# Kernel optimization log

Measured on AMD Instinct MI355X. Metric: run time of the kernel, lower is better.

## Reference

```python
import jax, jax.numpy as jnp
import numpy as np

N, H, E, G, OUT = 50000, 128, 600000, 256, 64
NUM_ITERS = 5
GAMMA = 0.1
EPS = 0.1
NEG_SLOPE = 0.01


def setup_inputs() -> dict:
    key = jax.random.key(0)
    ks = jax.random.split(key, 10)
    s = 1.0 / np.sqrt(H)
    x = jax.random.normal(ks[0], (N, H), dtype=jnp.float32)
    edge_index = jax.random.randint(ks[1], (2, E), 0, N, dtype=jnp.int64)
    batch = jnp.sort(jax.random.randint(ks[2], (N,), 0, G, dtype=jnp.int64))
    W = jax.random.normal(ks[3], (H, H), dtype=jnp.float32) * s
    bias = jax.random.normal(ks[4], (H,), dtype=jnp.float32) * s
    lin_w = jax.random.normal(ks[5], (H, H), dtype=jnp.float32) * s
    l1_w = jax.random.normal(ks[6], (3 * H // 2, 3 * H), dtype=jnp.float32) / np.sqrt(3 * H)
    l1_b = jax.random.normal(ks[7], (3 * H // 2,), dtype=jnp.float32) * 0.01
    l2_w = jax.random.normal(ks[8], (OUT, 3 * H // 2), dtype=jnp.float32) / np.sqrt(3 * H // 2)
    l2_b = jax.random.normal(ks[9], (OUT,), dtype=jnp.float32) * 0.01
    return {"x": x, "edge_index": edge_index, "batch": batch, "W": W, "bias": bias,
            "lin_w": lin_w, "l1_w": l1_w, "l1_b": l1_b, "l2_w": l2_w, "l2_b": l2_b}


def reference(x, edge_index, batch, W, bias, lin_w, l1_w, l1_b, l2_w, l2_b):
    n = x.shape[0]
    src, dst = edge_index[0], edge_index[1]
    # antisymmetric weight: W - W^T - gamma*I
    A = W - W.T - GAMMA * jnp.eye(W.shape[0], dtype=x.dtype)
    for _ in range(NUM_ITERS):
        neigh = x @ lin_w.T                                   # [N,H] linear (no bias)
        agg = jax.ops.segment_sum(neigh[src], dst, num_segments=n)  # gather-scatter add
        conv = x @ A.T + agg + bias
        x = x + EPS * jnp.tanh(conv)
    # triple global pooling per graph: add / max / mean
    add = jax.ops.segment_sum(x, batch, num_segments=G)
    mx = jax.ops.segment_max(x, batch, num_segments=G)
    cnt = jax.ops.segment_sum(jnp.ones((n,), dtype=x.dtype), batch, num_segments=G)
    safe_cnt = jnp.maximum(cnt, 1.0)[:, None]
    mean = add / safe_cnt
    mx = jnp.where(cnt[:, None] > 0, mx, 0.0)
    pooled = jnp.concatenate([add, mx, mean], axis=1)          # [G, 3H]
    h = jax.nn.leaky_relu(pooled @ l1_w.T + l1_b, NEG_SLOPE)
    out = jax.nn.leaky_relu(h @ l2_w.T + l2_b, NEG_SLOPE)
    return out
```

## Files before the change

kernel.cpp:

```cpp
#include <hip/hip_runtime.h>
#include <hip/hip_fp16.h>
#include <cmath>

#define H 128
#define GAMMA 0.1f
#define EPS 0.1f
#define NEG 0.01f
#define NGRAPH 256

typedef _Float16 half_t;
typedef _Float16 f16x8 __attribute__((ext_vector_type(8)));
typedef _Float16 f16x4 __attribute__((ext_vector_type(4)));
typedef _Float16 f16x2 __attribute__((ext_vector_type(2)));
typedef float f32x4 __attribute__((ext_vector_type(4)));

__device__ __forceinline__ float fast_tanh(float v) {
    float e = __builtin_amdgcn_exp2f(v * 2.8853900817779268f);
    float r = __builtin_amdgcn_rcpf(e + 1.0f);
    return 1.0f - 2.0f * r;
}

__global__ __launch_bounds__(256) void prep_cast_zero(
        const float* __restrict__ W, const float* __restrict__ lin_w,
        half_t* __restrict__ WtTf, const float* __restrict__ x,
        half_t* __restrict__ xh, int n4, int* __restrict__ deg, int N) {
    int stride = gridDim.x * 256;
    int tot = max(n4, max(32768, N));
    for (int i = blockIdx.x * 256 + threadIdx.x; i < tot; i += stride) {
        if (i < n4) {
            float4 v = *(const float4*)(x + (size_t)i * 4);
            half_t* o = xh + (size_t)i * 4;
            o[0] = (half_t)v.x; o[1] = (half_t)v.y; o[2] = (half_t)v.z; o[3] = (half_t)v.w;
        }
        if (i < 32768) {
            int t = i & 7;
            int lane = (i >> 3) & 63;
            int ct = (i >> 9) & 7;
            int s = i >> 12;
            int q = lane >> 4, m = lane & 15;
            int j = m * 8 + ct;
            int k = s * 32 + q * 8 + t;
            float v;
            if (k < H) v = W[j * H + k] - W[k * H + j] - (j == k ? GAMMA : 0.f);
            else       v = lin_w[j * H + (k - H)];
            WtTf[i] = (half_t)v;
        }
        if (i < N) deg[i] = 0;
    }
}

__global__ __launch_bounds__(256) void count_kernel(const int* __restrict__ dst,
                                                    int* __restrict__ deg, int E) {
    int stride = gridDim.x * 256;
    for (int e = blockIdx.x * 256 + threadIdx.x; e < E; e += stride)
        atomicAdd(&deg[dst[e]], 1);
}

#define SCHUNK 2048
__global__ __launch_bounds__(256) void scan_part(const int* __restrict__ deg,
                                                 int* __restrict__ partials, int N) {
    __shared__ int red[256];
    int t = threadIdx.x, b = blockIdx.x;
    int base = b * SCHUNK + t * 8;
    int s = 0;
#pragma unroll
    for (int i = 0; i < 8; ++i) { int idx = base + i; if (idx < N) s += deg[idx]; }
    red[t] = s;
    __syncthreads();
    for (int off = 128; off > 0; off >>= 1) {
        if (t < off) red[t] += red[t + off];
        __syncthreads();
    }
    if (t == 0) partials[b] = red[0];
}

__global__ void scan_mid(const int* __restrict__ partials, int* __restrict__ blkoff, int nblk) {
    int lane = threadIdx.x;
    int p = (lane < nblk) ? partials[lane] : 0;
    int v = p;
    for (int off = 1; off < 64; off <<= 1) {
        int u = __shfl_up(v, off);
        if (lane >= off) v += u;
    }
    if (lane < nblk) blkoff[lane] = v - p;
}

__global__ __launch_bounds__(256) void scan_final(const int* __restrict__ deg,
        const int* __restrict__ blkoff, int* __restrict__ row_start,
        int* __restrict__ cursor, int N, int E) {
    __shared__ int red[256];
    int t = threadIdx.x, b = blockIdx.x;
    int base = b * SCHUNK + t * 8;
    int v[8]; int s = 0;
#pragma unroll
    for (int i = 0; i < 8; ++i) { int idx = base + i; v[i] = (idx < N) ? deg[idx] : 0; s += v[i]; }
    red[t] = s;
    __syncthreads();
    for (int off = 1; off < 256; off <<= 1) {
        int u = (t >= off) ? red[t - off] : 0;
        __syncthreads();
        red[t] += u;
        __syncthreads();
    }
    int run = blkoff[b] + red[t] - s;
#pragma unroll
    for (int i = 0; i < 8; ++i) {
        int idx = base + i;
        if (idx < N) { row_start[idx] = run; cursor[idx] = run; run += v[i]; }
    }
    if (b == 0 && t == 0) row_start[N] = E;
}

__global__ __launch_bounds__(256) void fill_kernel(const int* __restrict__ src,
        const int* __restrict__ dst, int* __restrict__ cursor,
        int* __restrict__ csr_src, int E) {
    int stride = gridDim.x * 256;
    for (int e = blockIdx.x * 256 + threadIdx.x; e < E; e += stride) {
        int p = atomicAdd(&cursor[dst[e]], 1);
        csr_src[p] = src[e];
    }
}

__global__ __launch_bounds__(256) void gather_agg(const half_t* __restrict__ xh,
        const int* __restrict__ row_start, const int* __restrict__ csr_src,
        half_t* __restrict__ xaggh, int N) {
    int wid = __builtin_amdgcn_readfirstlane(blockIdx.x * 4 + (threadIdx.x >> 6));
    int nwaves = gridDim.x * 4;
    int lane = threadIdx.x & 63;
    for (int node = wid; node < N; node += nwaves) {
        int begin = row_start[node];
        int end   = row_start[node + 1];
        f16x2 accA = (f16x2){(half_t)0.f, (half_t)0.f};
        f16x2 accB = (f16x2){(half_t)0.f, (half_t)0.f};
        for (int base = begin; base < end; base += 64) {
            int cnt = min(64, end - base);
            int myidx = csr_src[base + min(lane, cnt - 1)];
            int j = 0;
            for (; j + 7 < cnt; j += 8) {
                int s0 = __builtin_amdgcn_readlane(myidx, j + 0);
                int s1 = __builtin_amdgcn_readlane(myidx, j + 1);
                int s2 = __builtin_amdgcn_readlane(myidx, j + 2);
                int s3 = __builtin_amdgcn_readlane(myidx, j + 3);
                int s4 = __builtin_amdgcn_readlane(myidx, j + 4);
                int s5 = __builtin_amdgcn_readlane(myidx, j + 5);
                int s6 = __builtin_amdgcn_readlane(myidx, j + 6);
                int s7 = __builtin_amdgcn_readlane(myidx, j + 7);
                f16x2 v0 = *(const f16x2*)(xh + (size_t)s0 * H + lane * 2);
                f16x2 v1 = *(const f16x2*)(xh + (size_t)s1 * H + lane * 2);
                f16x2 v2 = *(const f16x2*)(xh + (size_t)s2 * H + lane * 2);
                f16x2 v3 = *(const f16x2*)(xh + (size_t)s3 * H + lane * 2);
                f16x2 v4 = *(const f16x2*)(xh + (size_t)s4 * H + lane * 2);
                f16x2 v5 = *(const f16x2*)(xh + (size_t)s5 * H + lane * 2);
                f16x2 v6 = *(const f16x2*)(xh + (size_t)s6 * H + lane * 2);
                f16x2 v7 = *(const f16x2*)(xh + (size_t)s7 * H + lane * 2);
                accA += v0; accB += v1; accA += v2; accB += v3;
                accA += v4; accB += v5; accA += v6; accB += v7;
            }
            if (cnt - j >= 4) {
                int s0 = __builtin_amdgcn_readlane(myidx, j + 0);
                int s1 = __builtin_amdgcn_readlane(myidx, j + 1);
                int s2 = __builtin_amdgcn_readlane(myidx, j + 2);
                int s3 = __builtin_amdgcn_readlane(myidx, j + 3);
                f16x2 v0 = *(const f16x2*)(xh + (size_t)s0 * H + lane * 2);
                f16x2 v1 = *(const f16x2*)(xh + (size_t)s1 * H + lane * 2);
                f16x2 v2 = *(const f16x2*)(xh + (size_t)s2 * H + lane * 2);
                f16x2 v3 = *(const f16x2*)(xh + (size_t)s3 * H + lane * 2);
                accA += v0; accB += v1; accA += v2; accB += v3;
                j += 4;
            }
            int rem = cnt - j;
            if (rem > 0) {
                int s0 = __builtin_amdgcn_readlane(myidx, j);
                int s1 = __builtin_amdgcn_readlane(myidx, min(j + 1, cnt - 1));
                int s2 = __builtin_amdgcn_readlane(myidx, min(j + 2, cnt - 1));
                f16x2 v0 = *(const f16x2*)(xh + (size_t)s0 * H + lane * 2);
                f16x2 v1 = *(const f16x2*)(xh + (size_t)s1 * H + lane * 2);
                f16x2 v2 = *(const f16x2*)(xh + (size_t)s2 * H + lane * 2);
                accA += v0;
                if (rem > 1) accB += v1;
                if (rem > 2) accA += v2;
            }
        }
        f16x2 o = accA + accB;
        *(f16x2*)(xaggh + (size_t)node * H + lane * 2) = o;
    }
}

#define CROWS 64
__global__ __launch_bounds__(256) void conv_mfma(
        const half_t* __restrict__ xh, const half_t* __restrict__ xaggh,
        const half_t* __restrict__ WtTf, const float* __restrict__ bias,
        half_t* __restrict__ xhout, int N) {
    int tid = threadIdx.x;
    int wave = tid >> 6, lane = tid & 63;
    int q = lane >> 4, m = lane & 15;
    int n0 = blockIdx.x * CROWS + wave * 16;

    f32x4 acc[8];
#pragma unroll
    for (int ct = 0; ct < 8; ++ct) acc[ct] = (f32x4){0.f, 0.f, 0.f, 0.f};

    int arow = min(n0 + m, N - 1);
#pragma unroll
    for (int s = 0; s < 8; ++s) {
        f16x8 afrag = (s < 4)
            ? *(const f16x8*)(xh    + (size_t)arow * H + s * 32 + q * 8)
            : *(const f16x8*)(xaggh + (size_t)arow * H + (s - 4) * 32 + q * 8);
#pragma unroll
        for (int ct = 0; ct < 8; ++ct) {
            f16x8 bfrag = *(const f16x8*)(WtTf + ((s * 8 + ct) * 64 + lane) * 8);
            acc[ct] = __builtin_amdgcn_mfma_f32_16x16x32_f16(afrag, bfrag, acc[ct], 0, 0, 0);
        }
    }

    float4 b0 = *(const float4*)(bias + m * 8);
    float4 b1 = *(const float4*)(bias + m * 8 + 4);
    float bb[8] = {b0.x, b0.y, b0.z, b0.w, b1.x, b1.y, b1.z, b1.w};
#pragma unroll
    for (int r = 0; r < 4; ++r) {
        int row = n0 + q * 4 + r;
        if (row < N) {
            f16x8 xr = *(const f16x8*)(xh + (size_t)row * H + m * 8);
            f16x8 o;
#pragma unroll
            for (int ct = 0; ct < 8; ++ct) {
                float c = acc[ct][r] + bb[ct];
                o[ct] = (half_t)((float)xr[ct] + EPS * fast_tanh(c));
            }
            *(f16x8*)(xhout + (size_t)row * H + m * 8) = o;
        }
    }
}

__global__ __launch_bounds__(1024) void pool_mlp(const half_t* __restrict__ x,
        const int* __restrict__ batch,
        const float* __restrict__ l1_w, const float* __restrict__ l1_b,
        const float* __restrict__ l2_w, const float* __restrict__ l2_b,
        float* __restrict__ out, int N) {
    __shared__ float ssum[8][128];
    __shared__ float smax[8][128];
    __shared__ __align__(16) float sp[384];
    __shared__ __align__(16) float sh[192];
    int g = blockIdx.x, t = threadIdx.x;
    int feat = t & 127, slot = t >> 7;
    int lo = 0, hi = N;
    while (lo < hi) { int mid = (lo + hi) >> 1; if (batch[mid] < g) lo = mid + 1; else hi = mid; }
    int start = lo;
    hi = N;
    while (lo < hi) { int mid = (lo + hi) >> 1; if (batch[mid] < g + 1) lo = mid + 1; else hi = mid; }
    int end = lo;
    float sum = 0.f, mx = -INFINITY;
    for (int n = start + slot; n < end; n += 8) {
        float v = (float)x[(size_t)n * H + feat];
        sum += v;
        mx = fmaxf(mx, v);
    }
    ssum[slot][feat] = sum;
    smax[slot][feat] = mx;
    __syncthreads();
    if (t < 128) {
        float s = 0.f, m = -INFINITY;
#pragma unroll
        for (int k = 0; k < 8; ++k) { s += ssum[k][t]; m = fmaxf(m, smax[k][t]); }
        int cnt = end - start;
        sp[t] = s;
        sp[128 + t] = (cnt > 0) ? m : 0.f;
        sp[256 + t] = s / (float)(cnt > 0 ? cnt : 1);
    }
    __syncthreads();
    if (t < 192) {
        float acc = l1_b[t];
        const float* wr = l1_w + (size_t)t * 384;
        for (int k = 0; k < 384; k += 4) {
            float4 w = *(const float4*)(wr + k);
            float4 p = *(const float4*)(sp + k);
            acc += w.x * p.x + w.y * p.y + w.z * p.z + w.w * p.w;
        }
        sh[t] = acc > 0.f ? acc : NEG * acc;
    }
    __syncthreads();
    if (t < 64) {
        float acc = l2_b[t];
        const float* wr = l2_w + (size_t)t * 192;
        for (int k = 0; k < 192; k += 4) {
            float4 w = *(const float4*)(wr + k);
            float4 p = *(const float4*)(sh + k);
            acc += w.x * p.x + w.y * p.y + w.z * p.z + w.w * p.w;
        }
        out[g * 64 + t] = acc > 0.f ? acc : NEG * acc;
    }
}

extern "C" void kernel_launch(void* const* d_in, const int* in_sizes, int n_in,
                              void* d_out, int out_size, void* d_ws, size_t ws_size,
                              hipStream_t stream) {
    const float* x0    = (const float*)d_in[0];
    const int*   edge  = (const int*)d_in[1];
    const int*   batch = (const int*)d_in[2];
    const float* W     = (const float*)d_in[3];
    const float* bias  = (const float*)d_in[4];
    const float* lin_w = (const float*)d_in[5];
    const float* l1_w  = (const float*)d_in[6];
    const float* l1_b  = (const float*)d_in[7];
    const float* l2_w  = (const float*)d_in[8];
    const float* l2_b  = (const float*)d_in[9];
    float* out = (float*)d_out;

    int N = in_sizes[0] / H;
    int E = in_sizes[1] / 2;
    const int* src = edge;
    const int* dst = edge + E;

    size_t nh = (size_t)N * H;
    half_t* xhA    = (half_t*)d_ws;
    half_t* xhB    = xhA + nh;
    half_t* xaggh  = xhB + nh;
    half_t* WtTf   = xaggh + nh;
    int* deg       = (int*)(WtTf + 32768);
    int* row_start = deg + N;
    int* cursor    = row_start + N + 1;
    int* csr_src   = cursor + N;
    int* partials  = csr_src + E;
    int* blkoff    = partials + 64;

    int n4 = (int)(nh / 4);
    prep_cast_zero<<<1024, 256, 0, stream>>>(W, lin_w, WtTf, x0, xhA, n4, deg, N);

    count_kernel<<<1024, 256, 0, stream>>>(dst, deg, E);
    int nblk = (N + SCHUNK - 1) / SCHUNK;
    scan_part<<<nblk, 256, 0, stream>>>(deg, partials, N);
    scan_mid<<<1, 64, 0, stream>>>(partials, blkoff, nblk);
    scan_final<<<nblk, 256, 0, stream>>>(deg, blkoff, row_start, cursor, N, E);
    fill_kernel<<<1024, 256, 0, stream>>>(src, dst, cursor, csr_src, E);

    const half_t* xcur_h = xhA;
    int nblocks = (N + CROWS - 1) / CROWS;
    for (int it = 0; it < 5; ++it) {
        gather_agg<<<2048, 256, 0, stream>>>(xcur_h, row_start, csr_src, xaggh, N);
        half_t* xnext_h = (it & 1) ? xhA : xhB;
        conv_mfma<<<nblocks, 256, 0, stream>>>(xcur_h, xaggh, WtTf, bias, xnext_h, N);
        xcur_h = xnext_h;
    }

    pool_mlp<<<NGRAPH, 1024, 0, stream>>>(xcur_h, batch, l1_w, l1_b, l2_w, l2_b, out, N);
}
```

Measured before the change: 372.5 us.

## Fuse neighbor gather-aggregation into conv MFMA kernel via LDS staging

The separate gather_agg kernel is folded into the conv kernel. Each wave now aggregates neighbor rows for its own 16 nodes into a swizzled LDS tile, and the MFMA A-fragments for the aggregate half are read from that tile. This removes the global round trip for xaggh and one launch per iteration. In exchange, gather parallelism is tied to the conv grid of 782 blocks, with each wave processing its 16 nodes one after another, which may hide memory latency less well. Separately, the scan_mid kernel is removed and each scan_final block computes its own block offset with a wave reduction over the partials.

```diff
diff --git a/kernel.cpp b/kernel.cpp
--- a/kernel.cpp
+++ b/kernel.cpp
@@ -74,22 +74,17 @@
     if (t == 0) partials[b] = red[0];
 }
 
-__global__ void scan_mid(const int* __restrict__ partials, int* __restrict__ blkoff, int nblk) {
-    int lane = threadIdx.x;
-    int p = (lane < nblk) ? partials[lane] : 0;
-    int v = p;
-    for (int off = 1; off < 64; off <<= 1) {
-        int u = __shfl_up(v, off);
-        if (lane >= off) v += u;
-    }
-    if (lane < nblk) blkoff[lane] = v - p;
-}
-
 __global__ __launch_bounds__(256) void scan_final(const int* __restrict__ deg,
-        const int* __restrict__ blkoff, int* __restrict__ row_start,
+        const int* __restrict__ partials, int* __restrict__ row_start,
         int* __restrict__ cursor, int N, int E) {
     __shared__ int red[256];
+    __shared__ int s_boff;
     int t = threadIdx.x, b = blockIdx.x;
+    if (t < 64) {
+        int p = (t < b) ? partials[t] : 0;
+        for (int off = 32; off > 0; off >>= 1) p += __shfl_down(p, off);
+        if (t == 0) s_boff = p;
+    }
     int base = b * SCHUNK + t * 8;
     int v[8]; int s = 0;
 #pragma unroll
@@ -102,7 +97,7 @@
         red[t] += u;
         __syncthreads();
     }
-    int run = blkoff[b] + red[t] - s;
+    int run = s_boff + red[t] - s;
 #pragma unroll
     for (int i = 0; i < 8; ++i) {
         int idx = base + i;
@@ -121,80 +116,79 @@
     }
 }
 
-__global__ __launch_bounds__(256) void gather_agg(const half_t* __restrict__ xh,
+#define CROWS 64
+__global__ __launch_bounds__(256) void conv_fused(
+        const half_t* __restrict__ xh,
         const int* __restrict__ row_start, const int* __restrict__ csr_src,
-        half_t* __restrict__ xaggh, int N) {
-    int wid = __builtin_amdgcn_readfirstlane(blockIdx.x * 4 + (threadIdx.x >> 6));
-    int nwaves = gridDim.x * 4;
-    int lane = threadIdx.x & 63;
-    for (int node = wid; node < N; node += nwaves) {
-        int begin = row_start[node];
-        int end   = row_start[node + 1];
-        f16x2 accA = (f16x2){(half_t)0.f, (half_t)0.f};
-        f16x2 accB = (f16x2){(half_t)0.f, (half_t)0.f};
-        for (int base = begin; base < end; base += 64) {
-            int cnt = min(64, end - base);
-            int myidx = csr_src[base + min(lane, cnt - 1)];
-            int j = 0;
-            for (; j + 7 < cnt; j += 8) {
-                int s0 = __builtin_amdgcn_readlane(myidx, j + 0);
-                int s1 = __builtin_amdgcn_readlane(myidx, j + 1);
-                int s2 = __builtin_amdgcn_readlane(myidx, j + 2);
-                int s3 = __builtin_amdgcn_readlane(myidx, j + 3);
-                int s4 = __builtin_amdgcn_readlane(myidx, j + 4);
-                int s5 = __builtin_amdgcn_readlane(myidx, j + 5);
-                int s6 = __builtin_amdgcn_readlane(myidx, j + 6);
-                int s7 = __builtin_amdgcn_readlane(myidx, j + 7);
-                f16x2 v0 = *(const f16x2*)(xh + (size_t)s0 * H + lane * 2);
-                f16x2 v1 = *(const f16x2*)(xh + (size_t)s1 * H + lane * 2);
-                f16x2 v2 = *(const f16x2*)(xh + (size_t)s2 * H + lane * 2);
-                f16x2 v3 = *(const f16x2*)(xh + (size_t)s3 * H + lane * 2);
-                f16x2 v4 = *(const f16x2*)(xh + (size_t)s4 * H + lane * 2);
-                f16x2 v5 = *(const f16x2*)(xh + (size_t)s5 * H + lane * 2);
-                f16x2 v6 = *(const f16x2*)(xh + (size_t)s6 * H + lane * 2);
-                f16x2 v7 = *(const f16x2*)(xh + (size_t)s7 * H + lane * 2);
-                accA += v0; accB += v1; accA += v2; accB += v3;
-                accA += v4; accB += v5; accA += v6; accB += v7;
-            }
-            if (cnt - j >= 4) {
-                int s0 = __builtin_amdgcn_readlane(myidx, j + 0);
-                int s1 = __builtin_amdgcn_readlane(myidx, j + 1);
-                int s2 = __builtin_amdgcn_readlane(myidx, j + 2);
-                int s3 = __builtin_amdgcn_readlane(myidx, j + 3);
-                f16x2 v0 = *(const f16x2*)(xh + (size_t)s0 * H + lane * 2);
-                f16x2 v1 = *(const f16x2*)(xh + (size_t)s1 * H + lane * 2);
-                f16x2 v2 = *(const f16x2*)(xh + (size_t)s2 * H + lane * 2);
-                f16x2 v3 = *(const f16x2*)(xh + (size_t)s3 * H + lane * 2);
-                accA += v0; accB += v1; accA += v2; accB += v3;
-                j += 4;
-            }
-            int rem = cnt - j;
-            if (rem > 0) {
-                int s0 = __builtin_amdgcn_readlane(myidx, j);
-                int s1 = __builtin_amdgcn_readlane(myidx, min(j + 1, cnt - 1));
-                int s2 = __builtin_amdgcn_readlane(myidx, min(j + 2, cnt - 1));
-                f16x2 v0 = *(const f16x2*)(xh + (size_t)s0 * H + lane * 2);
-                f16x2 v1 = *(const f16x2*)(xh + (size_t)s1 * H + lane * 2);
-                f16x2 v2 = *(const f16x2*)(xh + (size_t)s2 * H + lane * 2);
-                accA += v0;
-                if (rem > 1) accB += v1;
-                if (rem > 2) accA += v2;
-            }
-        }
-        f16x2 o = accA + accB;
-        *(f16x2*)(xaggh + (size_t)node * H + lane * 2) = o;
-    }
-}
-
-#define CROWS 64
-__global__ __launch_bounds__(256) void conv_mfma(
-        const half_t* __restrict__ xh, const half_t* __restrict__ xaggh,
         const half_t* __restrict__ WtTf, const float* __restrict__ bias,
         half_t* __restrict__ xhout, int N) {
+    __shared__ __align__(16) char sagg[4][4096];
     int tid = threadIdx.x;
     int wave = tid >> 6, lane = tid & 63;
     int q = lane >> 4, m = lane & 15;
     int n0 = blockIdx.x * CROWS + wave * 16;
+    char* slds = sagg[wave];
+
+    for (int r = 0; r < 16; ++r) {
+        int node = n0 + r;
+        f16x2 accA = (f16x2){(half_t)0.f, (half_t)0.f};
+        f16x2 accB = (f16x2){(half_t)0.f, (half_t)0.f};
+        if (node < N) {
+            int begin = row_start[node];
+            int end   = row_start[node + 1];
+            for (int base = begin; base < end; base += 64) {
+                int cnt = min(64, end - base);
+                int myidx = csr_src[base + min(lane, cnt - 1)];
+                int j = 0;
+                for (; j + 7 < cnt; j += 8) {
+                    int s0 = __builtin_amdgcn_readlane(myidx, j + 0);
+                    int s1 = __builtin_amdgcn_readlane(myidx, j + 1);
+                    int s2 = __builtin_amdgcn_readlane(myidx, j + 2);
+                    int s3 = __builtin_amdgcn_readlane(myidx, j + 3);
+                    int s4 = __builtin_amdgcn_readlane(myidx, j + 4);
+                    int s5 = __builtin_amdgcn_readlane(myidx, j + 5);
+                    int s6 = __builtin_amdgcn_readlane(myidx, j + 6);
+                    int s7 = __builtin_amdgcn_readlane(myidx, j + 7);
+                    f16x2 v0 = *(const f16x2*)(xh + (size_t)s0 * H + lane * 2);
+                    f16x2 v1 = *(const f16x2*)(xh + (size_t)s1 * H + lane * 2);
+                    f16x2 v2 = *(const f16x2*)(xh + (size_t)s2 * H + lane * 2);
+                    f16x2 v3 = *(const f16x2*)(xh + (size_t)s3 * H + lane * 2);
+                    f16x2 v4 = *(const f16x2*)(xh + (size_t)s4 * H + lane * 2);
+                    f16x2 v5 = *(const f16x2*)(xh + (size_t)s5 * H + lane * 2);
+                    f16x2 v6 = *(const f16x2*)(xh + (size_t)s6 * H + lane * 2);
+                    f16x2 v7 = *(const f16x2*)(xh + (size_t)s7 * H + lane * 2);
+                    accA += v0; accB += v1; accA += v2; accB += v3;
+                    accA += v4; accB += v5; accA += v6; accB += v7;
+                }
+                if (cnt - j >= 4) {
+                    int s0 = __builtin_amdgcn_readlane(myidx, j + 0);
+                    int s1 = __builtin_amdgcn_readlane(myidx, j + 1);
+                    int s2 = __builtin_amdgcn_readlane(myidx, j + 2);
+                    int s3 = __builtin_amdgcn_readlane(myidx, j + 3);
+                    f16x2 v0 = *(const f16x2*)(xh + (size_t)s0 * H + lane * 2);
+                    f16x2 v1 = *(const f16x2*)(xh + (size_t)s1 * H + lane * 2);
+                    f16x2 v2 = *(const f16x2*)(xh + (size_t)s2 * H + lane * 2);
+                    f16x2 v3 = *(const f16x2*)(xh + (size_t)s3 * H + lane * 2);
+                    accA += v0; accB += v1; accA += v2; accB += v3;
+                    j += 4;
+                }
+                int rem = cnt - j;
+                if (rem > 0) {
+                    int s0 = __builtin_amdgcn_readlane(myidx, j);
+                    int s1 = __builtin_amdgcn_readlane(myidx, min(j + 1, cnt - 1));
+                    int s2 = __builtin_amdgcn_readlane(myidx, min(j + 2, cnt - 1));
+                    f16x2 v0 = *(const f16x2*)(xh + (size_t)s0 * H + lane * 2);
+                    f16x2 v1 = *(const f16x2*)(xh + (size_t)s1 * H + lane * 2);
+                    f16x2 v2 = *(const f16x2*)(xh + (size_t)s2 * H + lane * 2);
+                    accA += v0;
+                    if (rem > 1) accB += v1;
+                    if (rem > 2) accA += v2;
+                }
+            }
+        }
+        f16x2 o = accA + accB;
+        *(f16x2*)(slds + r * 256 + ((lane * 4) ^ ((r & 7) << 4))) = o;
+    }
 
     f32x4 acc[8];
 #pragma unroll
@@ -203,9 +197,13 @@
     int arow = min(n0 + m, N - 1);
 #pragma unroll
     for (int s = 0; s < 8; ++s) {
-        f16x8 afrag = (s < 4)
-            ? *(const f16x8*)(xh    + (size_t)arow * H + s * 32 + q * 8)
-            : *(const f16x8*)(xaggh + (size_t)arow * H + (s - 4) * 32 + q * 8);
+        f16x8 afrag;
+        if (s < 4) {
+            afrag = *(const f16x8*)(xh + (size_t)arow * H + s * 32 + q * 8);
+        } else {
+            afrag = *(const f16x8*)(slds + m * 256 +
+                                    ((((s - 4) * 64 + q * 16)) ^ ((m & 7) << 4)));
+        }
 #pragma unroll
         for (int ct = 0; ct < 8; ++ct) {
             f16x8 bfrag = *(const f16x8*)(WtTf + ((s * 8 + ct) * 64 + lane) * 8);
@@ -321,7 +319,6 @@
     int* cursor    = row_start + N + 1;
     int* csr_src   = cursor + N;
     int* partials  = csr_src + E;
-    int* blkoff    = partials + 64;
 
     int n4 = (int)(nh / 4);
     prep_cast_zero<<<1024, 256, 0, stream>>>(W, lin_w, WtTf, x0, xhA, n4, deg, N);
@@ -329,16 +326,15 @@
     count_kernel<<<1024, 256, 0, stream>>>(dst, deg, E);
     int nblk = (N + SCHUNK - 1) / SCHUNK;
     scan_part<<<nblk, 256, 0, stream>>>(deg, partials, N);
-    scan_mid<<<1, 64, 0, stream>>>(partials, blkoff, nblk);
-    scan_final<<<nblk, 256, 0, stream>>>(deg, blkoff, row_start, cursor, N, E);
+    scan_final<<<nblk, 256, 0, stream>>>(deg, partials, row_start, cursor, N, E);
     fill_kernel<<<1024, 256, 0, stream>>>(src, dst, cursor, csr_src, E);
 
     const half_t* xcur_h = xhA;
     int nblocks = (N + CROWS - 1) / CROWS;
     for (int it = 0; it < 5; ++it) {
-        gather_agg<<<2048, 256, 0, stream>>>(xcur_h, row_start, csr_src, xaggh, N);
         half_t* xnext_h = (it & 1) ? xhA : xhB;
-        conv_mfma<<<nblocks, 256, 0, stream>>>(xcur_h, xaggh, WtTf, bias, xnext_h, N);
+        conv_fused<<<nblocks, 256, 0, stream>>>(xcur_h, row_start, csr_src, WtTf,
+                                                bias, xnext_h, N);
         xcur_h = xnext_h;
     }
 
```

After: 389.4 us. 1.05x slower.
